# Kernel tuning notes

Hardware: AMD Instinct MI355X
Metric: run time of the kernel (lower is better)

The kernel has to match this reference:

```python
import jax, jax.numpy as jnp
import numpy as np

SEQ_LEN = 12
E = 64        # embedding_dim
H = 128       # h_dim
BNK = 1024    # bottleneck_dim
MLP = 1024    # mlp_dim
S, P = 32, 24 # scenes, peds per scene (uniform)
B = S * P


def setup_inputs() -> dict:
    key = jax.random.key(0)
    ks = jax.random.split(key, 24)
    w = lambda k, shape: jax.random.normal(k, shape, jnp.float32) * 0.05
    starts = jnp.arange(S, dtype=jnp.int32) * P
    return {
        'last_pos': jax.random.normal(ks[0], (B, 2), jnp.float32),
        'last_pos_rel': jax.random.normal(ks[1], (B, 2), jnp.float32),
        'h0': jax.random.normal(ks[2], (1, B, H), jnp.float32),
        'c0': jax.random.normal(ks[3], (1, B, H), jnp.float32),
        'seq_start_end': jnp.stack([starts, starts + P], axis=1),
        # decoder spatial embedding Linear(2, E)
        'W_se': w(ks[4], (2, E)), 'b_se': jnp.zeros((E,), jnp.float32),
        # LSTM (num_layers=1), PyTorch gate order i,f,g,o
        'W_ih': w(ks[5], (E, 4 * H)), 'b_ih': jnp.zeros((4 * H,), jnp.float32),
        'W_hh': w(ks[6], (H, 4 * H)), 'b_hh': jnp.zeros((4 * H,), jnp.float32),
        # hidden2pos Linear(H, 2)
        'W_hp': w(ks[7], (H, 2)), 'b_hp': jnp.zeros((2,), jnp.float32),
        # pool_net.spatial_embedding Linear(2, E)
        'W_pse': w(ks[8], (2, E)), 'b_pse': jnp.zeros((E,), jnp.float32),
        # pool_net.mlp_pre_pool [E+H, 512, BNK], ReLU, no batchnorm
        'W_p1': w(ks[9], (E + H, 512)), 'b_p1': jnp.zeros((512,), jnp.float32),
        'W_p2': w(ks[10], (512, BNK)), 'b_p2': jnp.zeros((BNK,), jnp.float32),
        # decoder.mlp [H+BNK, MLP, H], ReLU
        'W_m1': w(ks[11], (H + BNK, MLP)), 'b_m1': jnp.zeros((MLP,), jnp.float32),
        'W_m2': w(ks[12], (MLP, H)), 'b_m2': jnp.zeros((H,), jnp.float32),
    }


def reference(last_pos, last_pos_rel, h0, c0, seq_start_end,
              W_se, b_se, W_ih, b_ih, W_hh, b_hh, W_hp, b_hp,
              W_pse, b_pse, W_p1, b_p1, W_p2, b_p2, W_m1, b_m1, W_m2, b_m2):
    batch = last_pos.shape[0]
    n_scenes = seq_start_end.shape[0]
    peds = batch // n_scenes  # uniform scene sizes
    hdim = h0.shape[-1]

    dec_in0 = last_pos_rel @ W_se + b_se  # (B, E)

    def step(carry, _):
        lpos, dec_in, h, c = carry
        # single-step LSTM, PyTorch gate order i,f,g,o
        gates = dec_in @ W_ih + b_ih + h @ W_hh + b_hh  # (B, 4H)
        i, f, g, o = jnp.split(gates, 4, axis=-1)
        c_new = jax.nn.sigmoid(f) * c + jax.nn.sigmoid(i) * jnp.tanh(g)
        h_new = jax.nn.sigmoid(o) * jnp.tanh(c_new)
        rel_pos = h_new @ W_hp + b_hp            # (B, 2)
        curr_pos = rel_pos + lpos                # (B, 2)
        # --- PoolHiddenNet: pool_h[i] = max_j mlp([emb(pos_j - pos_i), h_j]) per scene ---
        pos = curr_pos.reshape(n_scenes, peds, 2)
        rel = pos[:, None, :, :] - pos[:, :, None, :]         # (S, Pi, Pj, 2), pos_j - pos_i
        emb = rel @ W_pse + b_pse                             # (S, Pi, Pj, E)
        hj = jnp.broadcast_to(h_new.reshape(n_scenes, 1, peds, hdim),
                              (n_scenes, peds, peds, hdim))   # h_j along axis 2
        x = jnp.concatenate([emb, hj], axis=-1)               # (S, Pi, Pj, E+H)
        x = jax.nn.relu(x @ W_p1 + b_p1)
        x = jax.nn.relu(x @ W_p2 + b_p2)                      # (S, Pi, Pj, BNK)
        pool_h = x.max(axis=2).reshape(batch, -1)             # (B, BNK)
        # --- decoder.mlp on [h, pool_h] -> new hidden state ---
        dh = jnp.concatenate([h_new, pool_h], axis=-1)
        dh = jax.nn.relu(dh @ W_m1 + b_m1)
        h_final = jax.nn.relu(dh @ W_m2 + b_m2)               # (B, H)
        dec_in_next = rel_pos @ W_se + b_se
        return (curr_pos, dec_in_next, h_final, c_new), rel_pos

    carry0 = (last_pos, dec_in0, h0[0], c0[0])
    (_, _, h_fin, _), pred_rel = jax.lax.scan(step, carry0, None, length=SEQ_LEN)
    return pred_rel, h_fin[None]  # (T, B, 2), (1, B, H)
```

## Files before the change

kernel.cpp:

```cpp
#include <hip/hip_runtime.h>
#include <math.h>

#define NB 768
#define NS 32
#define NP 24
#define ED 64
#define HD 128
#define G4 512
#define BNKD 1024
#define KM1 1152
#define TSTEPS 12
#define AR 4

typedef __bf16 bf16x8 __attribute__((ext_vector_type(8)));
typedef float f32x4 __attribute__((ext_vector_type(4)));
typedef unsigned short u16x8 __attribute__((ext_vector_type(8)));

__device__ __forceinline__ unsigned short f2bf(float f) {
  unsigned u = __float_as_uint(f);
  u = (u + 0x7FFFu + ((u >> 16) & 1u)) >> 16;
  return (unsigned short)u;
}
__device__ __forceinline__ unsigned pack2bf(float a, float b) {
  return (unsigned)f2bf(a) | ((unsigned)f2bf(b) << 16);
}
__device__ __forceinline__ float bf2f(unsigned short h) {
  return __uint_as_float(((unsigned)h) << 16);
}

__global__ void init_kernel(const float* __restrict__ last_pos,
                            const float* __restrict__ last_pos_rel,
                            const float* __restrict__ c0,
                            const float* __restrict__ W_se,
                            const float* __restrict__ b_se,
                            const float* __restrict__ W_pse,
                            const float* __restrict__ b_pse,
                            const float* __restrict__ W_p1,
                            const float* __restrict__ b_p1,
                            const float* __restrict__ W_p2,
                            const float* __restrict__ W_m1,
                            const float* __restrict__ W_m2,
                            float* __restrict__ ccar,
                            float* __restrict__ din, float* __restrict__ lpos,
                            float* __restrict__ Wc, float* __restrict__ bc,
                            unsigned short* __restrict__ W2T,
                            unsigned short* __restrict__ W1T,
                            unsigned short* __restrict__ WmT) {
  int stride = gridDim.x * blockDim.x;
  int idx0 = blockIdx.x * blockDim.x + threadIdx.x;
  for (int i = idx0; i < NB * HD; i += stride) ccar[i] = c0[i];
  for (int i = idx0; i < NB * 2; i += stride) lpos[i] = last_pos[i];
  for (int i = idx0; i < NB * ED; i += stride) {
    int r = i >> 6, e = i & 63;
    din[i] = b_se[e] + last_pos_rel[2 * r] * W_se[e]
                     + last_pos_rel[2 * r + 1] * W_se[ED + e];
  }
  for (int n = idx0; n < G4; n += stride) {
    float w0 = 0.f, w1 = 0.f, bb = b_p1[n];
    for (int e = 0; e < ED; ++e) {
      float wp = W_p1[e * G4 + n];
      w0 += W_pse[e] * wp;
      w1 += W_pse[ED + e] * wp;
      bb += b_pse[e] * wp;
    }
    Wc[n] = w0; Wc[G4 + n] = w1; bc[n] = bb;
  }
  for (int idx = idx0; idx < 1024 * 64; idx += stride) {
    int n = idx & 1023, k0 = (idx >> 10) << 3;
    unsigned pk0 = pack2bf(W_p2[(k0 + 0) * BNKD + n], W_p2[(k0 + 1) * BNKD + n]);
    unsigned pk1 = pack2bf(W_p2[(k0 + 2) * BNKD + n], W_p2[(k0 + 3) * BNKD + n]);
    unsigned pk2 = pack2bf(W_p2[(k0 + 4) * BNKD + n], W_p2[(k0 + 5) * BNKD + n]);
    unsigned pk3 = pack2bf(W_p2[(k0 + 6) * BNKD + n], W_p2[(k0 + 7) * BNKD + n]);
    *(uint4*)&W2T[n * G4 + k0] = make_uint4(pk0, pk1, pk2, pk3);
  }
  for (int idx = idx0; idx < 1024 * 144; idx += stride) {
    int n = idx & 1023, k0 = (idx >> 10) << 3;
    unsigned pk0 = pack2bf(W_m1[(k0 + 0) * BNKD + n], W_m1[(k0 + 1) * BNKD + n]);
    unsigned pk1 = pack2bf(W_m1[(k0 + 2) * BNKD + n], W_m1[(k0 + 3) * BNKD + n]);
    unsigned pk2 = pack2bf(W_m1[(k0 + 4) * BNKD + n], W_m1[(k0 + 5) * BNKD + n]);
    unsigned pk3 = pack2bf(W_m1[(k0 + 6) * BNKD + n], W_m1[(k0 + 7) * BNKD + n]);
    *(uint4*)&W1T[n * KM1 + k0] = make_uint4(pk0, pk1, pk2, pk3);
  }
  for (int idx = idx0; idx < 128 * 128; idx += stride) {
    int n = idx & 127, k0 = (idx >> 7) << 3;
    unsigned pk0 = pack2bf(W_m2[(k0 + 0) * HD + n], W_m2[(k0 + 1) * HD + n]);
    unsigned pk1 = pack2bf(W_m2[(k0 + 2) * HD + n], W_m2[(k0 + 3) * HD + n]);
    unsigned pk2 = pack2bf(W_m2[(k0 + 4) * HD + n], W_m2[(k0 + 5) * HD + n]);
    unsigned pk3 = pack2bf(W_m2[(k0 + 6) * HD + n], W_m2[(k0 + 7) * HD + n]);
    *(uint4*)&WmT[n * BNKD + k0] = make_uint4(pk0, pk1, pk2, pk3);
  }
}

__global__ __launch_bounds__(256) void step_a(
    const float* __restrict__ hprev, const float* __restrict__ cprev,
    const float* __restrict__ din, const float* __restrict__ lpos_in,
    const float* __restrict__ W_ih, const float* __restrict__ b_ih,
    const float* __restrict__ W_hh, const float* __restrict__ b_hh,
    const float* __restrict__ W_hp, const float* __restrict__ b_hp,
    const float* __restrict__ W_se, const float* __restrict__ b_se,
    const float* __restrict__ W_p1, const float* __restrict__ bc,
    const float* __restrict__ b_m2,
    float* __restrict__ hn, float* __restrict__ cnext,
    float* __restrict__ dnext, float* __restrict__ lpos_out,
    float* __restrict__ Hp1, float* __restrict__ pred_out,
    float* __restrict__ hacc_next, int relu_in) {
  __shared__ float x[AR][192];
  __shared__ float gg[AR][G4];
  __shared__ float hl[AR][HD];
  __shared__ float rp[AR][2];
  int t = threadIdx.x;
  int r0 = blockIdx.x * AR;

  for (int i = t; i < AR * ED; i += 256) { int r = i >> 6, k = i & 63; x[r][k] = din[(r0 + r) * ED + k]; }
  for (int i = t; i < AR * HD; i += 256) {
    int r = i >> 7, k = i & 127;
    float v = hprev[(r0 + r) * HD + k];
    if (relu_in) v = fmaxf(v, 0.f);
    x[r][ED + k] = v;
    hacc_next[(r0 + r) * HD + k] = b_m2[k];
  }
  __syncthreads();

  float acc[AR][2];
#pragma unroll
  for (int r = 0; r < AR; ++r) { acc[r][0] = b_ih[t] + b_hh[t]; acc[r][1] = b_ih[t + 256] + b_hh[t + 256]; }
  for (int k = 0; k < ED; ++k) {
    float w0 = W_ih[k * G4 + t], w1 = W_ih[k * G4 + t + 256];
#pragma unroll
    for (int r = 0; r < AR; ++r) { float a = x[r][k]; acc[r][0] += a * w0; acc[r][1] += a * w1; }
  }
  for (int k = 0; k < HD; ++k) {
    float w0 = W_hh[k * G4 + t], w1 = W_hh[k * G4 + t + 256];
#pragma unroll
    for (int r = 0; r < AR; ++r) { float a = x[r][ED + k]; acc[r][0] += a * w0; acc[r][1] += a * w1; }
  }
#pragma unroll
  for (int r = 0; r < AR; ++r) { gg[r][t] = acc[r][0]; gg[r][t + 256] = acc[r][1]; }
  __syncthreads();

  for (int i = t; i < AR * HD; i += 256) {
    int r = i >> 7, k = i & 127;
    float ig = gg[r][k], fg = gg[r][HD + k], gz = gg[r][2 * HD + k], og = gg[r][3 * HD + k];
    float si = 1.f / (1.f + expf(-ig));
    float sf = 1.f / (1.f + expf(-fg));
    float so = 1.f / (1.f + expf(-og));
    float gt = tanhf(gz);
    float c = sf * cprev[(r0 + r) * HD + k] + si * gt;
    float h = so * tanhf(c);
    cnext[(r0 + r) * HD + k] = c;
    hn[(r0 + r) * HD + k] = h;
    hl[r][k] = h;
  }
  __syncthreads();

  if (t < AR * 2) {
    int r = t >> 1, d = t & 1;
    float s = b_hp[d];
    for (int k = 0; k < HD; ++k) s += hl[r][k] * W_hp[k * 2 + d];
    rp[r][d] = s;
    pred_out[(r0 + r) * 2 + d] = s;
    lpos_out[(r0 + r) * 2 + d] = s + lpos_in[(r0 + r) * 2 + d];
  }
  __syncthreads();

  for (int i = t; i < AR * ED; i += 256) {
    int r = i >> 6, e = i & 63;
    dnext[(r0 + r) * ED + e] = b_se[e] + rp[r][0] * W_se[e] + rp[r][1] * W_se[ED + e];
  }

  float bc0 = bc[t], bc1 = bc[t + 256];
  float acc2[AR][2];
#pragma unroll
  for (int r = 0; r < AR; ++r) { acc2[r][0] = bc0; acc2[r][1] = bc1; }
  for (int k = 0; k < HD; ++k) {
    float w0 = W_p1[(ED + k) * G4 + t], w1 = W_p1[(ED + k) * G4 + t + 256];
#pragma unroll
    for (int r = 0; r < AR; ++r) { float a = hl[r][k]; acc2[r][0] += a * w0; acc2[r][1] += a * w1; }
  }
#pragma unroll
  for (int r = 0; r < AR; ++r) {
    Hp1[(r0 + r) * G4 + t] = acc2[r][0];
    Hp1[(r0 + r) * G4 + t + 256] = acc2[r][1];
  }
}

__global__ __launch_bounds__(256, 2) void pool_mfma(
    const float* __restrict__ curr_pos, const float* __restrict__ Hp1,
    const float* __restrict__ Wc,
    const unsigned short* __restrict__ W2T, const float* __restrict__ b_p2,
    float* __restrict__ pool_h) {
  __shared__ __align__(16) unsigned short Al[2][48 * 40];
  __shared__ float psx[NP], psy[NP], wc0[G4], wc1[G4];
  int t = threadIdx.x;
  int b = blockIdx.x;
  int s = b / 24, rem = b % 24;
  int ip = rem >> 1, nh = rem & 1;
  if (t < NP) {
    psx[t] = curr_pos[(s * NP + t) * 2];
    psy[t] = curr_pos[(s * NP + t) * 2 + 1];
  }
  for (int i = t; i < G4; i += 256) { wc0[i] = Wc[i]; wc1[i] = Wc[G4 + i]; }
  __syncthreads();

  int lane = t & 63, wn = t >> 6;
  int arow = lane & 15, ak = (lane >> 4) * 8;
  int kk2 = (t & 15) * 2;

  const float* hrow[3];
  float rxv[3], ryv[3];
  int awr[3];
#pragma unroll
  for (int p = 0; p < 3; ++p) {
    int m = p * 16 + (t >> 4);
    int j = m % 24, g = m / 24;
    hrow[p] = Hp1 + (size_t)(s * NP + j) * G4 + kk2;
    rxv[p] = psx[j] - psx[ip * 2 + g];
    ryv[p] = psy[j] - psy[ip * 2 + g];
    awr[p] = m * 40 + kk2;
  }
  int aoff[3];
#pragma unroll
  for (int f = 0; f < 3; ++f) aoff[f] = (f * 16 + arow) * 40 + ak;

  int n0 = nh * 512 + wn * 128;
  const unsigned short* bptr[8];
#pragma unroll
  for (int nf = 0; nf < 8; ++nf)
    bptr[nf] = W2T + (size_t)(n0 + nf * 16 + arow) * G4 + ak;

  f32x4 acc[3][8];
#pragma unroll
  for (int f = 0; f < 3; ++f)
#pragma unroll
    for (int nf = 0; nf < 8; ++nf) acc[f][nf] = (f32x4){0.f, 0.f, 0.f, 0.f};

  for (int kt = 0; kt < 16; ++kt) {
    int k0 = kt * 32;
    int k = k0 + kk2;
    float2 hv0 = *(const float2*)(hrow[0] + k0);
    float2 hv1 = *(const float2*)(hrow[1] + k0);
    float2 hv2 = *(const float2*)(hrow[2] + k0);
    bf16x8 bfr[8];
#pragma unroll
    for (int nf = 0; nf < 8; ++nf) bfr[nf] = *(const bf16x8*)(bptr[nf] + k0);

    float a0 = wc0[k], a1 = wc0[k + 1];
    float e0 = wc1[k], e1 = wc1[k + 1];
    unsigned short* dst = Al[kt & 1];
    {
      float v0 = fmaxf(hv0.x + a0 * rxv[0] + e0 * ryv[0], 0.f);
      float v1 = fmaxf(hv0.y + a1 * rxv[0] + e1 * ryv[0], 0.f);
      *(unsigned*)&dst[awr[0]] = pack2bf(v0, v1);
      v0 = fmaxf(hv1.x + a0 * rxv[1] + e0 * ryv[1], 0.f);
      v1 = fmaxf(hv1.y + a1 * rxv[1] + e1 * ryv[1], 0.f);
      *(unsigned*)&dst[awr[1]] = pack2bf(v0, v1);
      v0 = fmaxf(hv2.x + a0 * rxv[2] + e0 * ryv[2], 0.f);
      v1 = fmaxf(hv2.y + a1 * rxv[2] + e1 * ryv[2], 0.f);
      *(unsigned*)&dst[awr[2]] = pack2bf(v0, v1);
    }
    __syncthreads();
    bf16x8 af[3];
#pragma unroll
    for (int f = 0; f < 3; ++f) af[f] = *(const bf16x8*)&dst[aoff[f]];
#pragma unroll
    for (int nf = 0; nf < 8; ++nf)
#pragma unroll
      for (int f = 0; f < 3; ++f)
        acc[f][nf] = __builtin_amdgcn_mfma_f32_16x16x32_bf16(af[f], bfr[nf], acc[f][nf], 0, 0, 0);
  }

  int h = lane >> 4;
  int iA = s * NP + ip * 2;
#pragma unroll
  for (int nf = 0; nf < 8; ++nf) {
    f32x4 a0 = acc[0][nf], a1 = acc[1][nf], a2 = acc[2][nf];
    float v0 = fmaxf(fmaxf(a0[0], a0[1]), fmaxf(a0[2], a0[3]));
    float v1 = fmaxf(fmaxf(a1[0], a1[1]), fmaxf(a1[2], a1[3]));
    float v2 = fmaxf(fmaxf(a2[0], a2[1]), fmaxf(a2[2], a2[3]));
    v0 = fmaxf(v0, __shfl_xor(v0, 16));
    v1 = fmaxf(v1, __shfl_xor(v1, 16));
    v2 = fmaxf(v2, __shfl_xor(v2, 16));
    float xx = (h < 2) ? fmaxf(v0, v1) : v0;
    xx = fmaxf(xx, __shfl_xor(xx, 32));
    float yy = (h >= 2) ? fmaxf(v2, v1) : v2;
    yy = fmaxf(yy, __shfl_xor(yy, 32));
    int col = n0 + nf * 16 + (lane & 15);
    float bb = b_p2[col];
    xx = fmaxf(xx + bb, 0.f);
    yy = fmaxf(yy + bb, 0.f);
    if (h == 0) pool_h[(size_t)iA * BNKD + col] = xx;
    if (h == 1) pool_h[((size_t)iA + 1) * BNKD + col] = yy;
  }
}

__global__ __launch_bounds__(256) void mlp1_fused(
    const float* __restrict__ hn, const float* __restrict__ ph,
    const unsigned short* __restrict__ W1T, const float* __restrict__ b_m1,
    const unsigned short* __restrict__ WmT, float* __restrict__ hacc) {
  __shared__ __align__(16) float Pl[32][132];
  int t = threadIdx.x, b = blockIdx.x;
  int mt = b >> 3, nt = b & 7;
  int r0 = mt * 32, n0 = nt * 128;
  int lane = t & 63, wid = t >> 6, wm = wid >> 1, wn = wid & 1;
  int arow = lane & 15, ak = (lane >> 4) * 8;
  int h = lane >> 4;

  f32x4 acc0[4];
#pragma unroll
  for (int nf = 0; nf < 4; ++nf) acc0[nf] = (f32x4){0.f, 0.f, 0.f, 0.f};
  int mrow = r0 + wm * 16 + arow;
  const unsigned short* bp[4];
#pragma unroll
  for (int nf = 0; nf < 4; ++nf)
    bp[nf] = W1T + (size_t)(n0 + wn * 64 + nf * 16 + arow) * KM1 + ak;
  const float* arow_h = hn + (size_t)mrow * HD;
  const float* arow_p = ph + (size_t)mrow * BNKD - HD;

  for (int kt = 0; kt < 36; ++kt) {
    int kg = kt * 32 + ak;
    const float* src = (kg < HD) ? arow_h : arow_p;
    float4 v0 = *(const float4*)&src[kg];
    float4 v1 = *(const float4*)&src[kg + 4];
    u16x8 ua;
    ua[0] = f2bf(v0.x); ua[1] = f2bf(v0.y); ua[2] = f2bf(v0.z); ua[3] = f2bf(v0.w);
    ua[4] = f2bf(v1.x); ua[5] = f2bf(v1.y); ua[6] = f2bf(v1.z); ua[7] = f2bf(v1.w);
    bf16x8 a = __builtin_bit_cast(bf16x8, ua);
#pragma unroll
    for (int nf = 0; nf < 4; ++nf) {
      bf16x8 bb = *(const bf16x8*)(bp[nf] + kt * 32);
      acc0[nf] = __builtin_amdgcn_mfma_f32_16x16x32_bf16(a, bb, acc0[nf], 0, 0, 0);
    }
  }

#pragma unroll
  for (int nf = 0; nf < 4; ++nf) {
    int colp = wn * 64 + nf * 16 + arow;
    float bb = b_m1[n0 + colp];
#pragma unroll
    for (int rr = 0; rr < 4; ++rr)
      Pl[wm * 16 + h * 4 + rr][colp] = fmaxf(acc0[nf][rr] + bb, 0.f);
  }
  __syncthreads();

  f32x4 acc2[4];
#pragma unroll
  for (int nf = 0; nf < 4; ++nf) acc2[nf] = (f32x4){0.f, 0.f, 0.f, 0.f};
  const unsigned short* b2p[4];
#pragma unroll
  for (int nf = 0; nf < 4; ++nf)
    b2p[nf] = WmT + (size_t)(wn * 64 + nf * 16 + arow) * BNKD + n0 + ak;
  const float* prow = &Pl[wm * 16 + arow][0];

#pragma unroll
  for (int k2 = 0; k2 < 4; ++k2) {
    u16x8 uh, ul;
#pragma unroll
    for (int q = 0; q < 8; ++q) {
      float vv = prow[k2 * 32 + ak + q];
      unsigned short hh = f2bf(vv);
      uh[q] = hh;
      ul[q] = f2bf(vv - bf2f(hh));
    }
    bf16x8 ahi = __builtin_bit_cast(bf16x8, uh);
    bf16x8 alo = __builtin_bit_cast(bf16x8, ul);
#pragma unroll
    for (int nf = 0; nf < 4; ++nf) {
      bf16x8 bb = *(const bf16x8*)(b2p[nf] + k2 * 32);
      acc2[nf] = __builtin_amdgcn_mfma_f32_16x16x32_bf16(ahi, bb, acc2[nf], 0, 0, 0);
      acc2[nf] = __builtin_amdgcn_mfma_f32_16x16x32_bf16(alo, bb, acc2[nf], 0, 0, 0);
    }
  }
#pragma unroll
  for (int nf = 0; nf < 4; ++nf)
#pragma unroll
    for (int rr = 0; rr < 4; ++rr)
      atomicAdd(&hacc[(size_t)(r0 + wm * 16 + h * 4 + rr) * HD + wn * 64 + nf * 16 + arow],
                acc2[nf][rr]);
}

__global__ void final_h(const float* __restrict__ hacc, float* __restrict__ out) {
  int i = blockIdx.x * 256 + threadIdx.x;
  if (i < NB * HD) out[i] = fmaxf(hacc[i], 0.f);
}

extern "C" void kernel_launch(void* const* d_in, const int* in_sizes, int n_in,
                              void* d_out, int out_size, void* d_ws, size_t ws_size,
                              hipStream_t stream) {
  const float* last_pos     = (const float*)d_in[0];
  const float* last_pos_rel = (const float*)d_in[1];
  const float* h0   = (const float*)d_in[2];
  const float* c0   = (const float*)d_in[3];
  const float* W_se = (const float*)d_in[5];
  const float* b_se = (const float*)d_in[6];
  const float* W_ih = (const float*)d_in[7];
  const float* b_ih = (const float*)d_in[8];
  const float* W_hh = (const float*)d_in[9];
  const float* b_hh = (const float*)d_in[10];
  const float* W_hp = (const float*)d_in[11];
  const float* b_hp = (const float*)d_in[12];
  const float* W_pse = (const float*)d_in[13];
  const float* b_pse = (const float*)d_in[14];
  const float* W_p1 = (const float*)d_in[15];
  const float* b_p1 = (const float*)d_in[16];
  const float* W_p2 = (const float*)d_in[17];
  const float* b_p2 = (const float*)d_in[18];
  const float* W_m1 = (const float*)d_in[19];
  const float* b_m1 = (const float*)d_in[20];
  const float* W_m2 = (const float*)d_in[21];
  const float* b_m2 = (const float*)d_in[22];

  float* ws = (float*)d_ws;
  float* hacc[2]  = { ws,           ws + 98304 };
  float* ccar[2]  = { ws + 196608,  ws + 294912 };
  float* din[2]   = { ws + 393216,  ws + 442368 };
  float* lposb[2] = { ws + 491520,  ws + 493056 };
  float* hn   = ws + 494592;
  float* Hp1  = ws + 592896;
  float* ph   = ws + 986112;
  float* Wc   = ws + 1772544;
  float* bc   = ws + 1773568;
  unsigned short* W2T = (unsigned short*)(ws + 1774080);
  unsigned short* W1T = (unsigned short*)(ws + 2036224);
  unsigned short* WmT = (unsigned short*)(ws + 2626048);

  float* pred = (float*)d_out;

  init_kernel<<<128, 256, 0, stream>>>(last_pos, last_pos_rel, c0,
                                       W_se, b_se, W_pse, b_pse, W_p1, b_p1,
                                       W_p2, W_m1, W_m2,
                                       ccar[0], din[0], lposb[0],
                                       Wc, bc, W2T, W1T, WmT);

  for (int t = 0; t < TSTEPS; ++t) {
    int a = t & 1, b = (t + 1) & 1;
    step_a<<<NB / AR, 256, 0, stream>>>(
        t == 0 ? h0 : hacc[a], ccar[a], din[a], lposb[a],
        W_ih, b_ih, W_hh, b_hh, W_hp, b_hp, W_se, b_se, W_p1, bc, b_m2,
        hn, ccar[b], din[b], lposb[b], Hp1, pred + t * NB * 2,
        hacc[b], t == 0 ? 0 : 1);
    pool_mfma<<<NS * 24, 256, 0, stream>>>(lposb[b], Hp1, Wc, W2T, b_p2, ph);
    mlp1_fused<<<192, 256, 0, stream>>>(hn, ph, W1T, b_m1, WmT, hacc[b]);
  }

  final_h<<<384, 256, 0, stream>>>(hacc[0], (float*)d_out + TSTEPS * NB * 2);
}
```

Measured before the change: 1.389 ms.

## Move LSTM gate and pool-input GEMMs to split-bf16 MFMA, drop pool LDS staging

Replaces the scalar FP32 LSTM gate matmul and hidden-to-pool-layer-1 projection in step_a with MFMA bf16 GEMMs over 16 rows per block. To keep near-FP32 accuracy, weights and activations are split into hi and lo bf16 parts and combined with three MFMAs. The weight splits are pre-transposed in the init kernel. Separately, pool_mfma now builds its A fragments directly in registers from global Hp1 instead of staging through double-buffered LDS with a barrier, and drops the occupancy hint. This trades extra MFMA work and redundant global reads of Hp1 for fewer scalar FMAs and syncs.

```diff
diff --git a/kernel.cpp b/kernel.cpp
--- a/kernel.cpp
+++ b/kernel.cpp
@@ -9,8 +9,8 @@
 #define G4 512
 #define BNKD 1024
 #define KM1 1152
+#define KG 192
 #define TSTEPS 12
-#define AR 4
 
 typedef __bf16 bf16x8 __attribute__((ext_vector_type(8)));
 typedef float f32x4 __attribute__((ext_vector_type(4)));
@@ -40,12 +40,21 @@
                             const float* __restrict__ W_p2,
                             const float* __restrict__ W_m1,
                             const float* __restrict__ W_m2,
+                            const float* __restrict__ W_ih,
+                            const float* __restrict__ W_hh,
+                            const float* __restrict__ b_ih,
+                            const float* __restrict__ b_hh,
                             float* __restrict__ ccar,
                             float* __restrict__ din, float* __restrict__ lpos,
                             float* __restrict__ Wc, float* __restrict__ bc,
                             unsigned short* __restrict__ W2T,
                             unsigned short* __restrict__ W1T,
-                            unsigned short* __restrict__ WmT) {
+                            unsigned short* __restrict__ WmT,
+                            unsigned short* __restrict__ WgT_hi,
+                            unsigned short* __restrict__ WgT_lo,
+                            unsigned short* __restrict__ Wp1T_hi,
+                            unsigned short* __restrict__ Wp1T_lo,
+                            float* __restrict__ bg) {
   int stride = gridDim.x * blockDim.x;
   int idx0 = blockIdx.x * blockDim.x + threadIdx.x;
   for (int i = idx0; i < NB * HD; i += stride) ccar[i] = c0[i];
@@ -65,6 +74,7 @@
     }
     Wc[n] = w0; Wc[G4 + n] = w1; bc[n] = bb;
   }
+  for (int n = idx0; n < G4; n += stride) bg[n] = b_ih[n] + b_hh[n];
   for (int idx = idx0; idx < 1024 * 64; idx += stride) {
     int n = idx & 1023, k0 = (idx >> 10) << 3;
     unsigned pk0 = pack2bf(W_p2[(k0 + 0) * BNKD + n], W_p2[(k0 + 1) * BNKD + n]);
@@ -89,56 +99,127 @@
     unsigned pk3 = pack2bf(W_m2[(k0 + 6) * HD + n], W_m2[(k0 + 7) * HD + n]);
     *(uint4*)&WmT[n * BNKD + k0] = make_uint4(pk0, pk1, pk2, pk3);
   }
-}
-
-__global__ __launch_bounds__(256) void step_a(
+  for (int idx = idx0; idx < 512 * 24; idx += stride) {
+    int n = idx & 511, k0 = (idx >> 9) << 3;
+    unsigned short hi[8], lo[8];
+#pragma unroll
+    for (int q = 0; q < 8; ++q) {
+      int k = k0 + q;
+      float w = (k < ED) ? W_ih[k * G4 + n] : W_hh[(k - ED) * G4 + n];
+      unsigned short h = f2bf(w);
+      hi[q] = h;
+      lo[q] = f2bf(w - bf2f(h));
+    }
+    uint4 ph_, pl_;
+    ph_.x = hi[0] | (hi[1] << 16); ph_.y = hi[2] | (hi[3] << 16);
+    ph_.z = hi[4] | (hi[5] << 16); ph_.w = hi[6] | (hi[7] << 16);
+    pl_.x = lo[0] | (lo[1] << 16); pl_.y = lo[2] | (lo[3] << 16);
+    pl_.z = lo[4] | (lo[5] << 16); pl_.w = lo[6] | (lo[7] << 16);
+    *(uint4*)&WgT_hi[n * KG + k0] = ph_;
+    *(uint4*)&WgT_lo[n * KG + k0] = pl_;
+  }
+  for (int idx = idx0; idx < 512 * 16; idx += stride) {
+    int n = idx & 511, k0 = (idx >> 9) << 3;
+    unsigned short hi[8], lo[8];
+#pragma unroll
+    for (int q = 0; q < 8; ++q) {
+      float w = W_p1[(ED + k0 + q) * G4 + n];
+      unsigned short h = f2bf(w);
+      hi[q] = h;
+      lo[q] = f2bf(w - bf2f(h));
+    }
+    uint4 ph_, pl_;
+    ph_.x = hi[0] | (hi[1] << 16); ph_.y = hi[2] | (hi[3] << 16);
+    ph_.z = hi[4] | (hi[5] << 16); ph_.w = hi[6] | (hi[7] << 16);
+    pl_.x = lo[0] | (lo[1] << 16); pl_.y = lo[2] | (lo[3] << 16);
+    pl_.z = lo[4] | (lo[5] << 16); pl_.w = lo[6] | (lo[7] << 16);
+    *(uint4*)&Wp1T_hi[n * HD + k0] = ph_;
+    *(uint4*)&Wp1T_lo[n * HD + k0] = pl_;
+  }
+}
+
+__device__ __forceinline__ void split8(const float4 x0, const float4 x1,
+                                       bf16x8& ah, bf16x8& al) {
+  float v[8] = {x0.x, x0.y, x0.z, x0.w, x1.x, x1.y, x1.z, x1.w};
+#pragma unroll
+  for (int q = 0; q < 8; ++q) {
+    __bf16 h = (__bf16)v[q];
+    ah[q] = h;
+    al[q] = (__bf16)(v[q] - (float)h);
+  }
+}
+
+__global__ __launch_bounds__(256) void step_a_mfma(
     const float* __restrict__ hprev, const float* __restrict__ cprev,
     const float* __restrict__ din, const float* __restrict__ lpos_in,
-    const float* __restrict__ W_ih, const float* __restrict__ b_ih,
-    const float* __restrict__ W_hh, const float* __restrict__ b_hh,
+    const unsigned short* __restrict__ WgT_hi, const unsigned short* __restrict__ WgT_lo,
+    const float* __restrict__ bg,
+    const unsigned short* __restrict__ Wp1T_hi, const unsigned short* __restrict__ Wp1T_lo,
+    const float* __restrict__ bc,
     const float* __restrict__ W_hp, const float* __restrict__ b_hp,
     const float* __restrict__ W_se, const float* __restrict__ b_se,
-    const float* __restrict__ W_p1, const float* __restrict__ bc,
     const float* __restrict__ b_m2,
     float* __restrict__ hn, float* __restrict__ cnext,
     float* __restrict__ dnext, float* __restrict__ lpos_out,
     float* __restrict__ Hp1, float* __restrict__ pred_out,
     float* __restrict__ hacc_next, int relu_in) {
-  __shared__ float x[AR][192];
-  __shared__ float gg[AR][G4];
-  __shared__ float hl[AR][HD];
-  __shared__ float rp[AR][2];
+  __shared__ __align__(16) float xl[16][196];
+  __shared__ float gg[16][516];
+  __shared__ __align__(16) float hl[16][132];
+  __shared__ float rp[16][2];
   int t = threadIdx.x;
-  int r0 = blockIdx.x * AR;
-
-  for (int i = t; i < AR * ED; i += 256) { int r = i >> 6, k = i & 63; x[r][k] = din[(r0 + r) * ED + k]; }
-  for (int i = t; i < AR * HD; i += 256) {
+  int r0 = blockIdx.x * 16;
+
+  for (int i = t; i < 16 * ED; i += 256) { int r = i >> 6, k = i & 63; xl[r][k] = din[(r0 + r) * ED + k]; }
+  for (int i = t; i < 16 * HD; i += 256) {
     int r = i >> 7, k = i & 127;
     float v = hprev[(r0 + r) * HD + k];
     if (relu_in) v = fmaxf(v, 0.f);
-    x[r][ED + k] = v;
+    xl[r][ED + k] = v;
     hacc_next[(r0 + r) * HD + k] = b_m2[k];
   }
   __syncthreads();
 
-  float acc[AR][2];
-#pragma unroll
-  for (int r = 0; r < AR; ++r) { acc[r][0] = b_ih[t] + b_hh[t]; acc[r][1] = b_ih[t + 256] + b_hh[t + 256]; }
-  for (int k = 0; k < ED; ++k) {
-    float w0 = W_ih[k * G4 + t], w1 = W_ih[k * G4 + t + 256];
-#pragma unroll
-    for (int r = 0; r < AR; ++r) { float a = x[r][k]; acc[r][0] += a * w0; acc[r][1] += a * w1; }
-  }
-  for (int k = 0; k < HD; ++k) {
-    float w0 = W_hh[k * G4 + t], w1 = W_hh[k * G4 + t + 256];
-#pragma unroll
-    for (int r = 0; r < AR; ++r) { float a = x[r][ED + k]; acc[r][0] += a * w0; acc[r][1] += a * w1; }
-  }
-#pragma unroll
-  for (int r = 0; r < AR; ++r) { gg[r][t] = acc[r][0]; gg[r][t + 256] = acc[r][1]; }
+  int lane = t & 63, wn = t >> 6;
+  int arow = lane & 15, ak = (lane >> 4) * 8, h = lane >> 4;
+  int n0 = wn * 128;
+
+  f32x4 acc[8];
+#pragma unroll
+  for (int nf = 0; nf < 8; ++nf) acc[nf] = (f32x4){0.f, 0.f, 0.f, 0.f};
+  const unsigned short* bh[8];
+  const unsigned short* blp[8];
+#pragma unroll
+  for (int nf = 0; nf < 8; ++nf) {
+    bh[nf]  = WgT_hi + (size_t)(n0 + nf * 16 + arow) * KG + ak;
+    blp[nf] = WgT_lo + (size_t)(n0 + nf * 16 + arow) * KG + ak;
+  }
+#pragma unroll
+  for (int kt = 0; kt < 6; ++kt) {
+    float4 x0 = *(const float4*)&xl[arow][kt * 32 + ak];
+    float4 x1 = *(const float4*)&xl[arow][kt * 32 + ak + 4];
+    bf16x8 ah, al;
+    split8(x0, x1, ah, al);
+#pragma unroll
+    for (int nf = 0; nf < 8; ++nf) {
+      bf16x8 wh = *(const bf16x8*)(bh[nf] + kt * 32);
+      bf16x8 wl = *(const bf16x8*)(blp[nf] + kt * 32);
+      acc[nf] = __builtin_amdgcn_mfma_f32_16x16x32_bf16(ah, wh, acc[nf], 0, 0, 0);
+      acc[nf] = __builtin_amdgcn_mfma_f32_16x16x32_bf16(ah, wl, acc[nf], 0, 0, 0);
+      acc[nf] = __builtin_amdgcn_mfma_f32_16x16x32_bf16(al, wh, acc[nf], 0, 0, 0);
+    }
+  }
+#pragma unroll
+  for (int nf = 0; nf < 8; ++nf) {
+    int col = n0 + nf * 16 + arow;
+    float bb = bg[col];
+#pragma unroll
+    for (int rr = 0; rr < 4; ++rr)
+      gg[h * 4 + rr][col] = acc[nf][rr] + bb;
+  }
   __syncthreads();
 
-  for (int i = t; i < AR * HD; i += 256) {
+  for (int i = t; i < 16 * HD; i += 256) {
     int r = i >> 7, k = i & 127;
     float ig = gg[r][k], fg = gg[r][HD + k], gz = gg[r][2 * HD + k], og = gg[r][3 * HD + k];
     float si = 1.f / (1.f + expf(-ig));
@@ -146,51 +227,76 @@
     float so = 1.f / (1.f + expf(-og));
     float gt = tanhf(gz);
     float c = sf * cprev[(r0 + r) * HD + k] + si * gt;
-    float h = so * tanhf(c);
+    float hv = so * tanhf(c);
     cnext[(r0 + r) * HD + k] = c;
-    hn[(r0 + r) * HD + k] = h;
-    hl[r][k] = h;
+    hn[(r0 + r) * HD + k] = hv;
+    hl[r][k] = hv;
   }
   __syncthreads();
 
-  if (t < AR * 2) {
-    int r = t >> 1, d = t & 1;
-    float s = b_hp[d];
-    for (int k = 0; k < HD; ++k) s += hl[r][k] * W_hp[k * 2 + d];
-    rp[r][d] = s;
-    pred_out[(r0 + r) * 2 + d] = s;
-    lpos_out[(r0 + r) * 2 + d] = s + lpos_in[(r0 + r) * 2 + d];
+  {
+    int rr2 = t >> 4, d2 = (t >> 3) & 1, sub = t & 7;
+    float s = 0.f;
+#pragma unroll
+    for (int k2 = sub * 16; k2 < sub * 16 + 16; ++k2)
+      s += hl[rr2][k2] * W_hp[k2 * 2 + d2];
+    s += __shfl_xor(s, 1); s += __shfl_xor(s, 2); s += __shfl_xor(s, 4);
+    if (sub == 0) {
+      s += b_hp[d2];
+      rp[rr2][d2] = s;
+      pred_out[(r0 + rr2) * 2 + d2] = s;
+      lpos_out[(r0 + rr2) * 2 + d2] = s + lpos_in[(r0 + rr2) * 2 + d2];
+    }
   }
   __syncthreads();
 
-  for (int i = t; i < AR * ED; i += 256) {
+  for (int i = t; i < 16 * ED; i += 256) {
     int r = i >> 6, e = i & 63;
     dnext[(r0 + r) * ED + e] = b_se[e] + rp[r][0] * W_se[e] + rp[r][1] * W_se[ED + e];
   }
 
-  float bc0 = bc[t], bc1 = bc[t + 256];
-  float acc2[AR][2];
-#pragma unroll
-  for (int r = 0; r < AR; ++r) { acc2[r][0] = bc0; acc2[r][1] = bc1; }
-  for (int k = 0; k < HD; ++k) {
-    float w0 = W_p1[(ED + k) * G4 + t], w1 = W_p1[(ED + k) * G4 + t + 256];
-#pragma unroll
-    for (int r = 0; r < AR; ++r) { float a = hl[r][k]; acc2[r][0] += a * w0; acc2[r][1] += a * w1; }
-  }
-#pragma unroll
-  for (int r = 0; r < AR; ++r) {
-    Hp1[(r0 + r) * G4 + t] = acc2[r][0];
-    Hp1[(r0 + r) * G4 + t + 256] = acc2[r][1];
-  }
-}
-
-__global__ __launch_bounds__(256, 2) void pool_mfma(
+  f32x4 acc2[8];
+#pragma unroll
+  for (int nf = 0; nf < 8; ++nf) acc2[nf] = (f32x4){0.f, 0.f, 0.f, 0.f};
+  const unsigned short* ph_[8];
+  const unsigned short* pl_[8];
+#pragma unroll
+  for (int nf = 0; nf < 8; ++nf) {
+    ph_[nf] = Wp1T_hi + (size_t)(n0 + nf * 16 + arow) * HD + ak;
+    pl_[nf] = Wp1T_lo + (size_t)(n0 + nf * 16 + arow) * HD + ak;
+  }
+#pragma unroll
+  for (int kt = 0; kt < 4; ++kt) {
+    float4 x0 = *(const float4*)&hl[arow][kt * 32 + ak];
+    float4 x1 = *(const float4*)&hl[arow][kt * 32 + ak + 4];
+    bf16x8 ah, al;
+    split8(x0, x1, ah, al);
+#pragma unroll
+    for (int nf = 0; nf < 8; ++nf) {
+      bf16x8 wh = *(const bf16x8*)(ph_[nf] + kt * 32);
+      bf16x8 wl = *(const bf16x8*)(pl_[nf] + kt * 32);
+      acc2[nf] = __builtin_amdgcn_mfma_f32_16x16x32_bf16(ah, wh, acc2[nf], 0, 0, 0);
+      acc2[nf] = __builtin_amdgcn_mfma_f32_16x16x32_bf16(ah, wl, acc2[nf], 0, 0, 0);
+      acc2[nf] = __builtin_amdgcn_mfma_f32_16x16x32_bf16(al, wh, acc2[nf], 0, 0, 0);
+    }
+  }
+#pragma unroll
+  for (int nf = 0; nf < 8; ++nf) {
+    int col = n0 + nf * 16 + arow;
+    float bb = bc[col];
+#pragma unroll
+    for (int rr = 0; rr < 4; ++rr)
+      Hp1[(size_t)(r0 + h * 4 + rr) * G4 + col] = acc2[nf][rr] + bb;
+  }
+}
+
+__global__ __launch_bounds__(256) void pool_mfma(
     const float* __restrict__ curr_pos, const float* __restrict__ Hp1,
     const float* __restrict__ Wc,
     const unsigned short* __restrict__ W2T, const float* __restrict__ b_p2,
     float* __restrict__ pool_h) {
-  __shared__ __align__(16) unsigned short Al[2][48 * 40];
-  __shared__ float psx[NP], psy[NP], wc0[G4], wc1[G4];
+  __shared__ float psx[NP], psy[NP];
+  __shared__ __align__(16) float wc0[G4], wc1[G4];
   int t = threadIdx.x;
   int b = blockIdx.x;
   int s = b / 24, rem = b % 24;
@@ -204,29 +310,22 @@
 
   int lane = t & 63, wn = t >> 6;
   int arow = lane & 15, ak = (lane >> 4) * 8;
-  int kk2 = (t & 15) * 2;
-
-  const float* hrow[3];
-  float rxv[3], ryv[3];
-  int awr[3];
-#pragma unroll
-  for (int p = 0; p < 3; ++p) {
-    int m = p * 16 + (t >> 4);
+  int n0 = nh * 512 + wn * 128;
+
+  const float* hp[3];
+  float rx[3], ry[3];
+#pragma unroll
+  for (int f = 0; f < 3; ++f) {
+    int m = f * 16 + arow;
     int j = m % 24, g = m / 24;
-    hrow[p] = Hp1 + (size_t)(s * NP + j) * G4 + kk2;
-    rxv[p] = psx[j] - psx[ip * 2 + g];
-    ryv[p] = psy[j] - psy[ip * 2 + g];
-    awr[p] = m * 40 + kk2;
-  }
-  int aoff[3];
-#pragma unroll
-  for (int f = 0; f < 3; ++f) aoff[f] = (f * 16 + arow) * 40 + ak;
-
-  int n0 = nh * 512 + wn * 128;
-  const unsigned short* bptr[8];
+    hp[f] = Hp1 + (size_t)(s * NP + j) * G4 + ak;
+    rx[f] = psx[j] - psx[ip * 2 + g];
+    ry[f] = psy[j] - psy[ip * 2 + g];
+  }
+  const unsigned short* bp[8];
 #pragma unroll
   for (int nf = 0; nf < 8; ++nf)
-    bptr[nf] = W2T + (size_t)(n0 + nf * 16 + arow) * G4 + ak;
+    bp[nf] = W2T + (size_t)(n0 + nf * 16 + arow) * G4 + ak;
 
   f32x4 acc[3][8];
 #pragma unroll
@@ -234,34 +333,31 @@
 #pragma unroll
     for (int nf = 0; nf < 8; ++nf) acc[f][nf] = (f32x4){0.f, 0.f, 0.f, 0.f};
 
+#pragma unroll 2
   for (int kt = 0; kt < 16; ++kt) {
     int k0 = kt * 32;
-    int k = k0 + kk2;
-    float2 hv0 = *(const float2*)(hrow[0] + k0);
-    float2 hv1 = *(const float2*)(hrow[1] + k0);
-    float2 hv2 = *(const float2*)(hrow[2] + k0);
     bf16x8 bfr[8];
 #pragma unroll
-    for (int nf = 0; nf < 8; ++nf) bfr[nf] = *(const bf16x8*)(bptr[nf] + k0);
-
-    float a0 = wc0[k], a1 = wc0[k + 1];
-    float e0 = wc1[k], e1 = wc1[k + 1];
-    unsigned short* dst = Al[kt & 1];
-    {
-      float v0 = fmaxf(hv0.x + a0 * rxv[0] + e0 * ryv[0], 0.f);
-      float v1 = fmaxf(hv0.y + a1 * rxv[0] + e1 * ryv[0], 0.f);
-      *(unsigned*)&dst[awr[0]] = pack2bf(v0, v1);
-      v0 = fmaxf(hv1.x + a0 * rxv[1] + e0 * ryv[1], 0.f);
-      v1 = fmaxf(hv1.y + a1 * rxv[1] + e1 * ryv[1], 0.f);
-      *(unsigned*)&dst[awr[1]] = pack2bf(v0, v1);
-      v0 = fmaxf(hv2.x + a0 * rxv[2] + e0 * ryv[2], 0.f);
-      v1 = fmaxf(hv2.y + a1 * rxv[2] + e1 * ryv[2], 0.f);
-      *(unsigned*)&dst[awr[2]] = pack2bf(v0, v1);
-    }
-    __syncthreads();
+    for (int nf = 0; nf < 8; ++nf) bfr[nf] = *(const bf16x8*)(bp[nf] + k0);
+    float4 wa = *(const float4*)&wc0[k0 + ak];
+    float4 wb = *(const float4*)&wc0[k0 + ak + 4];
+    float4 va = *(const float4*)&wc1[k0 + ak];
+    float4 vb = *(const float4*)&wc1[k0 + ak + 4];
     bf16x8 af[3];
 #pragma unroll
-    for (int f = 0; f < 3; ++f) af[f] = *(const bf16x8*)&dst[aoff[f]];
+    for (int f = 0; f < 3; ++f) {
+      float4 h0 = *(const float4*)(hp[f] + k0);
+      float4 h1 = *(const float4*)(hp[f] + k0 + 4);
+      float rxf = rx[f], ryf = ry[f];
+      af[f][0] = (__bf16)fmaxf(h0.x + rxf * wa.x + ryf * va.x, 0.f);
+      af[f][1] = (__bf16)fmaxf(h0.y + rxf * wa.y + ryf * va.y, 0.f);
+      af[f][2] = (__bf16)fmaxf(h0.z + rxf * wa.z + ryf * va.z, 0.f);
+      af[f][3] = (__bf16)fmaxf(h0.w + rxf * wa.w + ryf * va.w, 0.f);
+      af[f][4] = (__bf16)fmaxf(h1.x + rxf * wb.x + ryf * vb.x, 0.f);
+      af[f][5] = (__bf16)fmaxf(h1.y + rxf * wb.y + ryf * vb.y, 0.f);
+      af[f][6] = (__bf16)fmaxf(h1.z + rxf * wb.z + ryf * vb.z, 0.f);
+      af[f][7] = (__bf16)fmaxf(h1.w + rxf * wb.w + ryf * vb.w, 0.f);
+    }
 #pragma unroll
     for (int nf = 0; nf < 8; ++nf)
 #pragma unroll
@@ -422,20 +518,27 @@
   unsigned short* W2T = (unsigned short*)(ws + 1774080);
   unsigned short* W1T = (unsigned short*)(ws + 2036224);
   unsigned short* WmT = (unsigned short*)(ws + 2626048);
+  unsigned short* WgT_hi  = (unsigned short*)(ws + 2691584);
+  unsigned short* WgT_lo  = (unsigned short*)(ws + 2740736);
+  unsigned short* Wp1T_hi = (unsigned short*)(ws + 2789888);
+  unsigned short* Wp1T_lo = (unsigned short*)(ws + 2822656);
+  float* bg = ws + 2855424;
 
   float* pred = (float*)d_out;
 
   init_kernel<<<128, 256, 0, stream>>>(last_pos, last_pos_rel, c0,
                                        W_se, b_se, W_pse, b_pse, W_p1, b_p1,
-                                       W_p2, W_m1, W_m2,
+                                       W_p2, W_m1, W_m2, W_ih, W_hh, b_ih, b_hh,
                                        ccar[0], din[0], lposb[0],
-                                       Wc, bc, W2T, W1T, WmT);
+                                       Wc, bc, W2T, W1T, WmT,
+                                       WgT_hi, WgT_lo, Wp1T_hi, Wp1T_lo, bg);
 
   for (int t = 0; t < TSTEPS; ++t) {
     int a = t & 1, b = (t + 1) & 1;
-    step_a<<<NB / AR, 256, 0, stream>>>(
+    step_a_mfma<<<NB / 16, 256, 0, stream>>>(
         t == 0 ? h0 : hacc[a], ccar[a], din[a], lposb[a],
-        W_ih, b_ih, W_hh, b_hh, W_hp, b_hp, W_se, b_se, W_p1, bc, b_m2,
+        WgT_hi, WgT_lo, bg, Wp1T_hi, Wp1T_lo, bc,
+        W_hp, b_hp, W_se, b_se, b_m2,
         hn, ccar[b], din[b], lposb[b], Hp1, pred + t * NB * 2,
         hacc[b], t == 0 ? 0 : 1);
     pool_mfma<<<NS * 24, 256, 0, stream>>>(lposb[b], Hp1, Wc, W2T, b_p2, ph);
```

After: 1.887 ms. 1.36x slower.

## Stage full pool A-tile in LDS upfront and drop per-iteration barriers

Applied to the files above, without the earlier changes.

The pool_mfma kernel now builds the whole 48x512 relu(Hp1 + rel·Wc) bf16 A tile in shared memory in a prologue, with padded rows, instead of producing a 32-wide slice each k-iteration behind double buffering and a __syncthreads. This takes barriers and activation math out of the MFMA loop. The loop is unrolled by 2 and launch bounds are raised to allow 3 blocks per CU. The cost is a much larger LDS footprint and a non-overlapped prologue. The 522-element row pitch leaves 16-byte vector LDS reads misaligned.

```diff
diff --git a/kernel.cpp b/kernel.cpp
--- a/kernel.cpp
+++ b/kernel.cpp
@@ -11,6 +11,7 @@
 #define KM1 1152
 #define TSTEPS 12
 #define AR 4
+#define PADW 522
 
 typedef __bf16 bf16x8 __attribute__((ext_vector_type(8)));
 typedef float f32x4 __attribute__((ext_vector_type(4)));
@@ -184,13 +185,13 @@
   }
 }
 
-__global__ __launch_bounds__(256, 2) void pool_mfma(
+__global__ __launch_bounds__(256, 3) void pool_mfma(
     const float* __restrict__ curr_pos, const float* __restrict__ Hp1,
     const float* __restrict__ Wc,
     const unsigned short* __restrict__ W2T, const float* __restrict__ b_p2,
     float* __restrict__ pool_h) {
-  __shared__ __align__(16) unsigned short Al[2][48 * 40];
-  __shared__ float psx[NP], psy[NP], wc0[G4], wc1[G4];
+  __shared__ __align__(16) unsigned short Al[48 * PADW];
+  __shared__ float psx[NP], psy[NP];
   int t = threadIdx.x;
   int b = blockIdx.x;
   int s = b / 24, rem = b % 24;
@@ -199,34 +200,43 @@
     psx[t] = curr_pos[(s * NP + t) * 2];
     psy[t] = curr_pos[(s * NP + t) * 2 + 1];
   }
-  for (int i = t; i < G4; i += 256) { wc0[i] = Wc[i]; wc1[i] = Wc[G4 + i]; }
+  __syncthreads();
+
+  {
+    int mq = t >> 4;
+    int q2 = (t & 15) * 2;
+#pragma unroll
+    for (int p = 0; p < 3; ++p) {
+      int m = p * 16 + mq;
+      int j = m % 24, g = m / 24;
+      float rx = psx[j] - psx[ip * 2 + g];
+      float ry = psy[j] - psy[ip * 2 + g];
+      const float* hr = Hp1 + (size_t)(s * NP + j) * G4;
+#pragma unroll 4
+      for (int c = 0; c < 16; ++c) {
+        int k = c * 32 + q2;
+        float2 hv = *(const float2*)&hr[k];
+        float2 wx = *(const float2*)&Wc[k];
+        float2 wy = *(const float2*)&Wc[G4 + k];
+        float v0 = fmaxf(hv.x + rx * wx.x + ry * wy.x, 0.f);
+        float v1 = fmaxf(hv.y + rx * wx.y + ry * wy.y, 0.f);
+        *(unsigned*)&Al[m * PADW + k] = pack2bf(v0, v1);
+      }
+    }
+  }
   __syncthreads();
 
   int lane = t & 63, wn = t >> 6;
   int arow = lane & 15, ak = (lane >> 4) * 8;
-  int kk2 = (t & 15) * 2;
-
-  const float* hrow[3];
-  float rxv[3], ryv[3];
-  int awr[3];
-#pragma unroll
-  for (int p = 0; p < 3; ++p) {
-    int m = p * 16 + (t >> 4);
-    int j = m % 24, g = m / 24;
-    hrow[p] = Hp1 + (size_t)(s * NP + j) * G4 + kk2;
-    rxv[p] = psx[j] - psx[ip * 2 + g];
-    ryv[p] = psy[j] - psy[ip * 2 + g];
-    awr[p] = m * 40 + kk2;
-  }
+  int n0 = nh * 512 + wn * 128;
+
+  const unsigned short* bp[8];
+#pragma unroll
+  for (int nf = 0; nf < 8; ++nf)
+    bp[nf] = W2T + (size_t)(n0 + nf * 16 + arow) * G4 + ak;
   int aoff[3];
 #pragma unroll
-  for (int f = 0; f < 3; ++f) aoff[f] = (f * 16 + arow) * 40 + ak;
-
-  int n0 = nh * 512 + wn * 128;
-  const unsigned short* bptr[8];
-#pragma unroll
-  for (int nf = 0; nf < 8; ++nf)
-    bptr[nf] = W2T + (size_t)(n0 + nf * 16 + arow) * G4 + ak;
+  for (int f = 0; f < 3; ++f) aoff[f] = (f * 16 + arow) * PADW + ak;
 
   f32x4 acc[3][8];
 #pragma unroll
@@ -234,34 +244,15 @@
 #pragma unroll
     for (int nf = 0; nf < 8; ++nf) acc[f][nf] = (f32x4){0.f, 0.f, 0.f, 0.f};
 
+#pragma unroll 2
   for (int kt = 0; kt < 16; ++kt) {
     int k0 = kt * 32;
-    int k = k0 + kk2;
-    float2 hv0 = *(const float2*)(hrow[0] + k0);
-    float2 hv1 = *(const float2*)(hrow[1] + k0);
-    float2 hv2 = *(const float2*)(hrow[2] + k0);
     bf16x8 bfr[8];
 #pragma unroll
-    for (int nf = 0; nf < 8; ++nf) bfr[nf] = *(const bf16x8*)(bptr[nf] + k0);
-
-    float a0 = wc0[k], a1 = wc0[k + 1];
-    float e0 = wc1[k], e1 = wc1[k + 1];
-    unsigned short* dst = Al[kt & 1];
-    {
-      float v0 = fmaxf(hv0.x + a0 * rxv[0] + e0 * ryv[0], 0.f);
-      float v1 = fmaxf(hv0.y + a1 * rxv[0] + e1 * ryv[0], 0.f);
-      *(unsigned*)&dst[awr[0]] = pack2bf(v0, v1);
-      v0 = fmaxf(hv1.x + a0 * rxv[1] + e0 * ryv[1], 0.f);
-      v1 = fmaxf(hv1.y + a1 * rxv[1] + e1 * ryv[1], 0.f);
-      *(unsigned*)&dst[awr[1]] = pack2bf(v0, v1);
-      v0 = fmaxf(hv2.x + a0 * rxv[2] + e0 * ryv[2], 0.f);
-      v1 = fmaxf(hv2.y + a1 * rxv[2] + e1 * ryv[2], 0.f);
-      *(unsigned*)&dst[awr[2]] = pack2bf(v0, v1);
-    }
-    __syncthreads();
+    for (int nf = 0; nf < 8; ++nf) bfr[nf] = *(const bf16x8*)(bp[nf] + k0);
     bf16x8 af[3];
 #pragma unroll
-    for (int f = 0; f < 3; ++f) af[f] = *(const bf16x8*)&dst[aoff[f]];
+    for (int f = 0; f < 3; ++f) af[f] = *(const bf16x8*)&Al[aoff[f] + k0];
 #pragma unroll
     for (int nf = 0; nf < 8; ++nf)
 #pragma unroll
```

Result: slower. 1.468 ms (+5.7%).
